# Kernel optimization log

Measured on AMD Instinct MI355X. Metric: run time of the kernel, lower is better.

Reference implementation:

```python
import jax, jax.numpy as jnp
import numpy as np

HIDDEN_DIM = 2048
NUM_EXPERTS = 8
TOP_K = 2
SCORE_SCALE_FACTOR = 1.0
TOKENS = 8192  # batch_size in the original 2D input


def setup_inputs() -> dict:
    key = jax.random.key(0)
    k1, k2, k3 = jax.random.split(key, 3)
    hidden_states = jax.random.normal(k1, (TOKENS, HIDDEN_DIM), dtype=jnp.float32)
    # nn.Linear weights (out_features, in_features), Kaiming-uniform-like scale
    gate_w = jax.random.normal(k2, (NUM_EXPERTS, HIDDEN_DIM), dtype=jnp.float32) / np.float32(np.sqrt(HIDDEN_DIM))
    expert_w = jax.random.normal(k3, (NUM_EXPERTS, HIDDEN_DIM, HIDDEN_DIM), dtype=jnp.float32) / np.float32(np.sqrt(HIDDEN_DIM))
    return {"hidden_states": hidden_states, "gate_w": gate_w, "expert_w": expert_w}


def reference(hidden_states, gate_w, expert_w):
    # router: logits = x @ W_gate^T, softmax in float32 (matches F.softmax(dtype=torch.float))
    router_logits = hidden_states @ gate_w.T                      # [T, E]
    routing_probs = jax.nn.softmax(router_logits.astype(jnp.float32), axis=-1)
    top_w, top_i = jax.lax.top_k(routing_probs, TOP_K)            # [T, K]
    top_w = top_w / jnp.sum(top_w, axis=-1, keepdims=True)        # renormalize over top-k
    top_w = top_w.astype(hidden_states.dtype)

    T = hidden_states.shape[0]
    # dense combine weights [T, E]: zero for unselected experts -> exactly the
    # gather-GEMM-scatter math (full capacity, no dropped tokens)
    combine = jnp.zeros((T, NUM_EXPERTS), dtype=hidden_states.dtype)
    combine = combine.at[jnp.arange(T)[:, None], top_i].set(top_w)

    # out[t,h] = scale * sum_e combine[t,e] * (x[t,:] @ expert_w[e]^T)[h]
    final_hidden_states = jnp.einsum('td,ehd,te->th', hidden_states, expert_w, combine) * SCORE_SCALE_FACTOR
    return final_hidden_states, router_logits
```

## Files before the change

kernel.cpp:

```cpp
#include <hip/hip_runtime.h>
#include <hip/hip_bf16.h>
#include <stdint.h>

#define TOKENS 8192
#define HD     2048
#define NE     8

typedef __attribute__((ext_vector_type(8)))  short short8;
typedef __attribute__((ext_vector_type(8)))  unsigned short ushort8v;
typedef __attribute__((ext_vector_type(4)))  float f32x4;
typedef __attribute__((ext_vector_type(16))) float f32x16;

__device__ __forceinline__ unsigned short f2bf_rne(float f) {
  union { float f; unsigned u; } v; v.f = f;
  unsigned u = v.u;
  return (unsigned short)((u + 0x7fffu + ((u >> 16) & 1u)) >> 16);
}

__device__ __forceinline__ void async_load16(const void* g, void* lds) {
  __builtin_amdgcn_global_load_lds(
      (const __attribute__((address_space(1))) unsigned int*)g,
      (__attribute__((address_space(3))) unsigned int*)lds, 16, 0, 0);
}

__global__ __launch_bounds__(256) void prep_kernel(
    const float* __restrict__ x, const float* __restrict__ gw,
    const float* __restrict__ ew, unsigned short* __restrict__ xb,
    unsigned short* __restrict__ wb, float* __restrict__ logits_out,
    int* __restrict__ counts, int* __restrict__ btok,
    float* __restrict__ bwt) {
  if (blockIdx.x >= 2048) {
    int i = (blockIdx.x - 2048) * 256 + threadIdx.x;
    const int n8 = NE * HD * HD / 8;
    const int stride = 4096 * 256;
    const float4* s4 = (const float4*)ew;
    ushort8v* d8 = (ushort8v*)wb;
    for (; i < n8; i += stride) {
      float4 a = s4[i * 2], b = s4[i * 2 + 1];
      ushort8v o;
      o[0] = f2bf_rne(a.x); o[1] = f2bf_rne(a.y);
      o[2] = f2bf_rne(a.z); o[3] = f2bf_rne(a.w);
      o[4] = f2bf_rne(b.x); o[5] = f2bf_rne(b.y);
      o[6] = f2bf_rne(b.z); o[7] = f2bf_rne(b.w);
      d8[i] = o;
    }
    return;
  }
  const int wid  = threadIdx.x >> 6;
  const int lane = threadIdx.x & 63;
  const int t = blockIdx.x * 4 + wid;

  const float4* xr = (const float4*)(x + (size_t)t * HD);
  const float4* g4 = (const float4*)gw;
  ushort4* xb4 = (ushort4*)(xb + (size_t)t * HD);

  float acc[NE];
#pragma unroll
  for (int e = 0; e < NE; ++e) acc[e] = 0.f;

#pragma unroll
  for (int it = 0; it < 8; ++it) {
    int idx = it * 64 + lane;
    float4 v = xr[idx];
    ushort4 o;
    o.x = f2bf_rne(v.x); o.y = f2bf_rne(v.y);
    o.z = f2bf_rne(v.z); o.w = f2bf_rne(v.w);
    xb4[idx] = o;
#pragma unroll
    for (int e = 0; e < NE; ++e) {
      float4 g = g4[e * 512 + idx];
      acc[e] += v.x * g.x + v.y * g.y + v.z * g.z + v.w * g.w;
    }
  }
#pragma unroll
  for (int e = 0; e < NE; ++e) {
#pragma unroll
    for (int off = 32; off > 0; off >>= 1)
      acc[e] += __shfl_xor(acc[e], off, 64);
  }
  if (lane == 0) {
    float* lo = logits_out + (size_t)t * NE;
#pragma unroll
    for (int e = 0; e < NE; ++e) lo[e] = acc[e];
    int i0 = 0; float b0 = acc[0];
#pragma unroll
    for (int k = 1; k < NE; ++k) if (acc[k] > b0) { b0 = acc[k]; i0 = k; }
    int i1 = -1; float b1 = -3.4e38f;
#pragma unroll
    for (int k = 0; k < NE; ++k) if (k != i0 && acc[k] > b1) { b1 = acc[k]; i1 = k; }
    float w0 = 1.f / (1.f + __expf(b1 - b0));
    float w1 = 1.f - w0;
    int p0 = atomicAdd(&counts[i0 * 32], 1);
    btok[i0 * TOKENS + p0] = t;
    bwt [i0 * TOKENS + p0] = w0;
    int p1 = atomicAdd(&counts[i1 * 32], 1);
    btok[i1 * TOKENS + p1] = t | (1 << 13);
    bwt [i1 * TOKENS + p1] = w1;
  }
}

__global__ __launch_bounds__(256, 4) void moe_gemm_kernel(
    const unsigned short* __restrict__ xb,
    const unsigned short* __restrict__ wb,
    const int* __restrict__ counts,
    const int* __restrict__ btok,
    const float* __restrict__ bwt,
    float* __restrict__ out,
    unsigned short* __restrict__ slot1) {
  int d = blockIdx.x;
  int e, coltile, rowtile;
  if (d < 2048) {
    e       = d & 7;
    rowtile = (d >> 3) & 15;
    coltile = d >> 7;
  } else {
    int u = d - 2048;
    e       = u & 7;
    coltile = (u & 127) >> 3;
    rowtile = 16 + (u >> 7);
  }
  const int cnt = counts[e * 32];
  if (rowtile * 128 >= cnt) return;

  __shared__ unsigned short As[128 * 64];
  __shared__ unsigned short Bs[128 * 64];

  const int tid  = threadIdx.x;
  const int wid  = tid >> 6;
  const int lane = tid & 63;

  int a_off[4], b_off[4];
#pragma unroll
  for (int it = 0; it < 4; ++it) {
    int slot = wid * 256 + it * 64 + lane;
    int row  = slot >> 3;
    int ch   = (slot & 7) ^ (row & 7);
    int rc   = rowtile * 128 + row;
    rc = rc < cnt ? rc : cnt - 1;
    a_off[it] = (btok[e * TOKENS + rc] & (TOKENS - 1)) * HD + ch * 8;
    b_off[it] = (e * HD + coltile * 128 + row) * HD + ch * 8;
  }

  f32x16 acc[2][2];
#pragma unroll
  for (int i = 0; i < 2; ++i)
#pragma unroll
    for (int j = 0; j < 2; ++j)
#pragma unroll
      for (int r = 0; r < 16; ++r) acc[i][j][r] = 0.f;

  const int l5  = lane >> 5;
  const int ln  = lane & 31;
  const int wm2 = wid >> 1;
  const int wn2 = wid & 1;

  int a_rd[2][4], b_rd[2][4];
#pragma unroll
  for (int t = 0; t < 2; ++t)
#pragma unroll
    for (int kc = 0; kc < 4; ++kc) {
      int ra = wm2 * 64 + t * 32 + ln;
      a_rd[t][kc] = ra * 64 + ((kc * 2 + l5) ^ (ra & 7)) * 8;
      int rb = wn2 * 64 + t * 32 + ln;
      b_rd[t][kc] = rb * 64 + ((kc * 2 + l5) ^ (rb & 7)) * 8;
    }

  for (int k0 = 0; k0 < HD; k0 += 64) {
#pragma unroll
    for (int it = 0; it < 4; ++it) {
      async_load16(xb + a_off[it] + k0, &As[(wid * 256 + it * 64) * 8]);
      async_load16(wb + b_off[it] + k0, &Bs[(wid * 256 + it * 64) * 8]);
    }
    __syncthreads();
    short8 fa[2][4], fb[2][4];
#pragma unroll
    for (int t = 0; t < 2; ++t)
#pragma unroll
      for (int kc = 0; kc < 4; ++kc) {
        fa[t][kc] = *(const short8*)&As[a_rd[t][kc]];
        fb[t][kc] = *(const short8*)&Bs[b_rd[t][kc]];
      }
#pragma unroll
    for (int kc = 0; kc < 4; ++kc)
#pragma unroll
      for (int i = 0; i < 2; ++i)
#pragma unroll
        for (int j = 0; j < 2; ++j)
          acc[i][j] = __builtin_amdgcn_mfma_f32_32x32x16_bf16(
              fa[i][kc], fb[j][kc], acc[i][j], 0, 0, 0);
    __syncthreads();
  }

#pragma unroll
  for (int ti = 0; ti < 2; ++ti)
#pragma unroll
    for (int rg = 0; rg < 16; ++rg) {
      int row = (rg & 3) + 8 * (rg >> 2) + 4 * l5;
      int gm  = rowtile * 128 + wm2 * 64 + ti * 32 + row;
      if (gm < cnt) {
        int   dv = btok[e * TOKENS + gm];
        float w  = bwt [e * TOKENS + gm];
        int   nb = coltile * 128 + wn2 * 64 + ln;
        float v0 = w * acc[ti][0][rg];
        float v1 = w * acc[ti][1][rg];
        if (dv < TOKENS) {
          float* orow = out + (size_t)dv * HD + nb;
          orow[0]  = v0;
          orow[32] = v1;
        } else {
          unsigned short* srow = slot1 + (size_t)(dv - TOKENS) * HD + nb;
          srow[0]  = f2bf_rne(v0);
          srow[32] = f2bf_rne(v1);
        }
      }
    }
}

__global__ __launch_bounds__(256) void combine_kernel(
    const unsigned short* __restrict__ s1, float* __restrict__ out) {
  size_t u = (size_t)blockIdx.x * 256 + threadIdx.x;
  ushort8v sv = ((const ushort8v*)s1)[u];
  float4* o = (float4*)out + u * 2;
  float4 a = o[0], b = o[1];
  a.x += __uint_as_float((unsigned)sv[0] << 16);
  a.y += __uint_as_float((unsigned)sv[1] << 16);
  a.z += __uint_as_float((unsigned)sv[2] << 16);
  a.w += __uint_as_float((unsigned)sv[3] << 16);
  b.x += __uint_as_float((unsigned)sv[4] << 16);
  b.y += __uint_as_float((unsigned)sv[5] << 16);
  b.z += __uint_as_float((unsigned)sv[6] << 16);
  b.w += __uint_as_float((unsigned)sv[7] << 16);
  o[0] = a; o[1] = b;
}

extern "C" void kernel_launch(void* const* d_in, const int* in_sizes, int n_in,
                              void* d_out, int out_size, void* d_ws, size_t ws_size,
                              hipStream_t stream) {
  const float* x  = (const float*)d_in[0];
  const float* gw = (const float*)d_in[1];
  const float* ew = (const float*)d_in[2];
  float* out = (float*)d_out;

  char* ws = (char*)d_ws;
  unsigned short* xb    = (unsigned short*)ws;
  unsigned short* wb    = (unsigned short*)(ws + 33554432u);
  unsigned short* slot1 = (unsigned short*)(ws + 100663296u);
  int*   counts = (int*)(ws + 134217728u);
  int*   btok   = (int*)(ws + 134218752u);
  float* bwt    = (float*)(ws + 134480896u);

  float* logits = out + (size_t)TOKENS * HD;

  hipMemsetAsync(counts, 0, 1024, stream);
  prep_kernel<<<6144, 256, 0, stream>>>(x, gw, ew, xb, wb, logits,
                                        counts, btok, bwt);
  moe_gemm_kernel<<<4096, 256, 0, stream>>>(xb, wb, counts, btok, bwt, out, slot1);
  combine_kernel<<<8192, 256, 0, stream>>>(slot1, out);
}
```

Baseline: 483.2 us.

## Group tokens by expert pair so one block computes both experts and combines

Tokens are now bucketed by their unordered top-2 expert pair (28 buckets) rather than by single expert. Each GEMM block loads one A tile and two expert weight tiles, runs both MFMA chains and writes the weighted sum directly. This removes the bf16 slot buffer, its rounding, and the separate combine pass. The cost is smaller, less balanced buckets with more partially filled row tiles, twice the accumulator registers (occupancy hint lowered to 2), and weight tiles re-read across more buckets.

```diff
diff --git a/kernel.cpp b/kernel.cpp
--- a/kernel.cpp
+++ b/kernel.cpp
@@ -5,11 +5,15 @@
 #define TOKENS 8192
 #define HD     2048
 #define NE     8
+#define NP     28
+#define PCAP   8192
 
 typedef __attribute__((ext_vector_type(8)))  short short8;
 typedef __attribute__((ext_vector_type(8)))  unsigned short ushort8v;
-typedef __attribute__((ext_vector_type(4)))  float f32x4;
 typedef __attribute__((ext_vector_type(16))) float f32x16;
+
+__constant__ int d_pa[NP] = {0,0,0,0,0,0,0,1,1,1,1,1,1,2,2,2,2,2,3,3,3,3,4,4,4,5,5,6};
+__constant__ int d_pb[NP] = {1,2,3,4,5,6,7,2,3,4,5,6,7,3,4,5,6,7,4,5,6,7,5,6,7,6,7,7};
 
 __device__ __forceinline__ unsigned short f2bf_rne(float f) {
   union { float f; unsigned u; } v; v.f = f;
@@ -28,7 +32,7 @@
     const float* __restrict__ ew, unsigned short* __restrict__ xb,
     unsigned short* __restrict__ wb, float* __restrict__ logits_out,
     int* __restrict__ counts, int* __restrict__ btok,
-    float* __restrict__ bwt) {
+    float2* __restrict__ bw2) {
   if (blockIdx.x >= 2048) {
     int i = (blockIdx.x - 2048) * 256 + threadIdx.x;
     const int n8 = NE * HD * HD / 8;
@@ -90,64 +94,60 @@
     for (int k = 0; k < NE; ++k) if (k != i0 && acc[k] > b1) { b1 = acc[k]; i1 = k; }
     float w0 = 1.f / (1.f + __expf(b1 - b0));
     float w1 = 1.f - w0;
-    int p0 = atomicAdd(&counts[i0 * 32], 1);
-    btok[i0 * TOKENS + p0] = t;
-    bwt [i0 * TOKENS + p0] = w0;
-    int p1 = atomicAdd(&counts[i1 * 32], 1);
-    btok[i1 * TOKENS + p1] = t | (1 << 13);
-    bwt [i1 * TOKENS + p1] = w1;
-  }
-}
-
-__global__ __launch_bounds__(256, 4) void moe_gemm_kernel(
+    int a  = i0 < i1 ? i0 : i1;
+    int b  = i0 < i1 ? i1 : i0;
+    float wa = i0 < i1 ? w0 : w1;
+    float wbv = i0 < i1 ? w1 : w0;
+    int p = a * (13 - a) / 2 + b - 1;
+    int pos = atomicAdd(&counts[p * 32], 1);
+    btok[p * PCAP + pos] = t;
+    bw2 [p * PCAP + pos] = make_float2(wa, wbv);
+  }
+}
+
+__global__ __launch_bounds__(256, 2) void moe_gemm_kernel(
     const unsigned short* __restrict__ xb,
     const unsigned short* __restrict__ wb,
     const int* __restrict__ counts,
     const int* __restrict__ btok,
-    const float* __restrict__ bwt,
-    float* __restrict__ out,
-    unsigned short* __restrict__ slot1) {
-  int d = blockIdx.x;
-  int e, coltile, rowtile;
-  if (d < 2048) {
-    e       = d & 7;
-    rowtile = (d >> 3) & 15;
-    coltile = d >> 7;
-  } else {
-    int u = d - 2048;
-    e       = u & 7;
-    coltile = (u & 127) >> 3;
-    rowtile = 16 + (u >> 7);
-  }
-  const int cnt = counts[e * 32];
-  if (rowtile * 128 >= cnt) return;
-
-  __shared__ unsigned short As[128 * 64];
-  __shared__ unsigned short Bs[128 * 64];
+    const float2* __restrict__ bw2,
+    float* __restrict__ out) {
+  const int d = blockIdx.x;
+  const int p = d >> 8;
+  const int r = (d >> 4) & 15;
+  const int c = d & 15;
+  const int cnt = counts[p * 32];
+  if (r * 128 >= cnt) return;
+  const int ea = d_pa[p], eb = d_pb[p];
+
+  __shared__ unsigned short As [128 * 64];
+  __shared__ unsigned short B0s[128 * 64];
+  __shared__ unsigned short B1s[128 * 64];
 
   const int tid  = threadIdx.x;
   const int wid  = tid >> 6;
   const int lane = tid & 63;
 
-  int a_off[4], b_off[4];
+  int a_off[4], b0_off[4], b1_off[4];
 #pragma unroll
   for (int it = 0; it < 4; ++it) {
     int slot = wid * 256 + it * 64 + lane;
     int row  = slot >> 3;
     int ch   = (slot & 7) ^ (row & 7);
-    int rc   = rowtile * 128 + row;
+    int rc   = r * 128 + row;
     rc = rc < cnt ? rc : cnt - 1;
-    a_off[it] = (btok[e * TOKENS + rc] & (TOKENS - 1)) * HD + ch * 8;
-    b_off[it] = (e * HD + coltile * 128 + row) * HD + ch * 8;
-  }
-
-  f32x16 acc[2][2];
+    a_off[it]  = btok[p * PCAP + rc] * HD + ch * 8;
+    b0_off[it] = (ea * HD + c * 128 + row) * HD + ch * 8;
+    b1_off[it] = (eb * HD + c * 128 + row) * HD + ch * 8;
+  }
+
+  f32x16 accA[2][2], accB[2][2];
 #pragma unroll
   for (int i = 0; i < 2; ++i)
 #pragma unroll
     for (int j = 0; j < 2; ++j)
 #pragma unroll
-      for (int r = 0; r < 16; ++r) acc[i][j][r] = 0.f;
+      for (int g = 0; g < 16; ++g) { accA[i][j][g] = 0.f; accB[i][j][g] = 0.f; }
 
   const int l5  = lane >> 5;
   const int ln  = lane & 31;
@@ -168,26 +168,29 @@
   for (int k0 = 0; k0 < HD; k0 += 64) {
 #pragma unroll
     for (int it = 0; it < 4; ++it) {
-      async_load16(xb + a_off[it] + k0, &As[(wid * 256 + it * 64) * 8]);
-      async_load16(wb + b_off[it] + k0, &Bs[(wid * 256 + it * 64) * 8]);
+      int lb = (wid * 256 + it * 64) * 8;
+      async_load16(xb + a_off[it]  + k0, &As [lb]);
+      async_load16(wb + b0_off[it] + k0, &B0s[lb]);
+      async_load16(wb + b1_off[it] + k0, &B1s[lb]);
     }
     __syncthreads();
-    short8 fa[2][4], fb[2][4];
-#pragma unroll
-    for (int t = 0; t < 2; ++t)
-#pragma unroll
-      for (int kc = 0; kc < 4; ++kc) {
-        fa[t][kc] = *(const short8*)&As[a_rd[t][kc]];
-        fb[t][kc] = *(const short8*)&Bs[b_rd[t][kc]];
-      }
-#pragma unroll
-    for (int kc = 0; kc < 4; ++kc)
-#pragma unroll
-      for (int i = 0; i < 2; ++i)
-#pragma unroll
-        for (int j = 0; j < 2; ++j)
-          acc[i][j] = __builtin_amdgcn_mfma_f32_32x32x16_bf16(
-              fa[i][kc], fb[j][kc], acc[i][j], 0, 0, 0);
+#pragma unroll
+    for (int kc = 0; kc < 4; ++kc) {
+      short8 a0 = *(const short8*)&As[a_rd[0][kc]];
+      short8 a1 = *(const short8*)&As[a_rd[1][kc]];
+      short8 f0 = *(const short8*)&B0s[b_rd[0][kc]];
+      short8 f1 = *(const short8*)&B0s[b_rd[1][kc]];
+      accA[0][0] = __builtin_amdgcn_mfma_f32_32x32x16_bf16(a0, f0, accA[0][0], 0, 0, 0);
+      accA[0][1] = __builtin_amdgcn_mfma_f32_32x32x16_bf16(a0, f1, accA[0][1], 0, 0, 0);
+      accA[1][0] = __builtin_amdgcn_mfma_f32_32x32x16_bf16(a1, f0, accA[1][0], 0, 0, 0);
+      accA[1][1] = __builtin_amdgcn_mfma_f32_32x32x16_bf16(a1, f1, accA[1][1], 0, 0, 0);
+      short8 g0 = *(const short8*)&B1s[b_rd[0][kc]];
+      short8 g1 = *(const short8*)&B1s[b_rd[1][kc]];
+      accB[0][0] = __builtin_amdgcn_mfma_f32_32x32x16_bf16(a0, g0, accB[0][0], 0, 0, 0);
+      accB[0][1] = __builtin_amdgcn_mfma_f32_32x32x16_bf16(a0, g1, accB[0][1], 0, 0, 0);
+      accB[1][0] = __builtin_amdgcn_mfma_f32_32x32x16_bf16(a1, g0, accB[1][0], 0, 0, 0);
+      accB[1][1] = __builtin_amdgcn_mfma_f32_32x32x16_bf16(a1, g1, accB[1][1], 0, 0, 0);
+    }
     __syncthreads();
   }
 
@@ -196,41 +199,18 @@
 #pragma unroll
     for (int rg = 0; rg < 16; ++rg) {
       int row = (rg & 3) + 8 * (rg >> 2) + 4 * l5;
-      int gm  = rowtile * 128 + wm2 * 64 + ti * 32 + row;
+      int gm  = r * 128 + wm2 * 64 + ti * 32 + row;
       if (gm < cnt) {
-        int   dv = btok[e * TOKENS + gm];
-        float w  = bwt [e * TOKENS + gm];
-        int   nb = coltile * 128 + wn2 * 64 + ln;
-        float v0 = w * acc[ti][0][rg];
-        float v1 = w * acc[ti][1][rg];
-        if (dv < TOKENS) {
-          float* orow = out + (size_t)dv * HD + nb;
-          orow[0]  = v0;
-          orow[32] = v1;
-        } else {
-          unsigned short* srow = slot1 + (size_t)(dv - TOKENS) * HD + nb;
-          srow[0]  = f2bf_rne(v0);
-          srow[32] = f2bf_rne(v1);
-        }
+        int    tok = btok[p * PCAP + gm];
+        float2 w   = bw2 [p * PCAP + gm];
+        int    nb  = c * 128 + wn2 * 64 + ln;
+        float v0 = w.x * accA[ti][0][rg] + w.y * accB[ti][0][rg];
+        float v1 = w.x * accA[ti][1][rg] + w.y * accB[ti][1][rg];
+        float* orow = out + (size_t)tok * HD + nb;
+        orow[0]  = v0;
+        orow[32] = v1;
       }
     }
-}
-
-__global__ __launch_bounds__(256) void combine_kernel(
-    const unsigned short* __restrict__ s1, float* __restrict__ out) {
-  size_t u = (size_t)blockIdx.x * 256 + threadIdx.x;
-  ushort8v sv = ((const ushort8v*)s1)[u];
-  float4* o = (float4*)out + u * 2;
-  float4 a = o[0], b = o[1];
-  a.x += __uint_as_float((unsigned)sv[0] << 16);
-  a.y += __uint_as_float((unsigned)sv[1] << 16);
-  a.z += __uint_as_float((unsigned)sv[2] << 16);
-  a.w += __uint_as_float((unsigned)sv[3] << 16);
-  b.x += __uint_as_float((unsigned)sv[4] << 16);
-  b.y += __uint_as_float((unsigned)sv[5] << 16);
-  b.z += __uint_as_float((unsigned)sv[6] << 16);
-  b.w += __uint_as_float((unsigned)sv[7] << 16);
-  o[0] = a; o[1] = b;
 }
 
 extern "C" void kernel_launch(void* const* d_in, const int* in_sizes, int n_in,
@@ -242,18 +222,16 @@
   float* out = (float*)d_out;
 
   char* ws = (char*)d_ws;
-  unsigned short* xb    = (unsigned short*)ws;
-  unsigned short* wb    = (unsigned short*)(ws + 33554432u);
-  unsigned short* slot1 = (unsigned short*)(ws + 100663296u);
-  int*   counts = (int*)(ws + 134217728u);
-  int*   btok   = (int*)(ws + 134218752u);
-  float* bwt    = (float*)(ws + 134480896u);
+  unsigned short* xb   = (unsigned short*)ws;
+  unsigned short* wb   = (unsigned short*)(ws + 33554432u);
+  int*    btok   = (int*)   (ws + 100663296u);
+  float2* bw2    = (float2*)(ws + 101580800u);
+  int*    counts = (int*)   (ws + 103415808u);
 
   float* logits = out + (size_t)TOKENS * HD;
 
-  hipMemsetAsync(counts, 0, 1024, stream);
+  hipMemsetAsync(counts, 0, NP * 32 * sizeof(int), stream);
   prep_kernel<<<6144, 256, 0, stream>>>(x, gw, ew, xb, wb, logits,
-                                        counts, btok, bwt);
-  moe_gemm_kernel<<<4096, 256, 0, stream>>>(xb, wb, counts, btok, bwt, out, slot1);
-  combine_kernel<<<8192, 256, 0, stream>>>(slot1, out);
-}
+                                        counts, btok, bw2);
+  moe_gemm_kernel<<<NP * 256, 256, 0, stream>>>(xb, wb, counts, btok, bw2, out);
+}
```

Result: slower. 533.9 us (+10.5%).

## Replace bf16 slot buffer and combine pass with atomic fp32 scatter-add

Applied to the files above, without the earlier changes.

Drops the second-slot bf16 staging buffer and the separate combine kernel. Output is zeroed with a memset and the GEMM epilogue does atomicAdd of weighted results straight into fp32 out. Routing and bucketing move into a new bucket_kernel that uses wave ballot plus prefix count, so there is one atomic per wave instead of one per token. This trades the combine kernel's read and write traffic for a 64MB memset and about 33M float atomics, and it adds an extra launch.

```diff
diff --git a/kernel.cpp b/kernel.cpp
--- a/kernel.cpp
+++ b/kernel.cpp
@@ -8,7 +8,6 @@
 
 typedef __attribute__((ext_vector_type(8)))  short short8;
 typedef __attribute__((ext_vector_type(8)))  unsigned short ushort8v;
-typedef __attribute__((ext_vector_type(4)))  float f32x4;
 typedef __attribute__((ext_vector_type(16))) float f32x16;
 
 __device__ __forceinline__ unsigned short f2bf_rne(float f) {
@@ -26,9 +25,7 @@
 __global__ __launch_bounds__(256) void prep_kernel(
     const float* __restrict__ x, const float* __restrict__ gw,
     const float* __restrict__ ew, unsigned short* __restrict__ xb,
-    unsigned short* __restrict__ wb, float* __restrict__ logits_out,
-    int* __restrict__ counts, int* __restrict__ btok,
-    float* __restrict__ bwt) {
+    unsigned short* __restrict__ wb, float* __restrict__ logits_out) {
   if (blockIdx.x >= 2048) {
     int i = (blockIdx.x - 2048) * 256 + threadIdx.x;
     const int n8 = NE * HD * HD / 8;
@@ -82,20 +79,39 @@
     float* lo = logits_out + (size_t)t * NE;
 #pragma unroll
     for (int e = 0; e < NE; ++e) lo[e] = acc[e];
-    int i0 = 0; float b0 = acc[0];
-#pragma unroll
-    for (int k = 1; k < NE; ++k) if (acc[k] > b0) { b0 = acc[k]; i0 = k; }
-    int i1 = -1; float b1 = -3.4e38f;
-#pragma unroll
-    for (int k = 0; k < NE; ++k) if (k != i0 && acc[k] > b1) { b1 = acc[k]; i1 = k; }
-    float w0 = 1.f / (1.f + __expf(b1 - b0));
-    float w1 = 1.f - w0;
-    int p0 = atomicAdd(&counts[i0 * 32], 1);
-    btok[i0 * TOKENS + p0] = t;
-    bwt [i0 * TOKENS + p0] = w0;
-    int p1 = atomicAdd(&counts[i1 * 32], 1);
-    btok[i1 * TOKENS + p1] = t | (1 << 13);
-    bwt [i1 * TOKENS + p1] = w1;
+  }
+}
+
+__global__ __launch_bounds__(256) void bucket_kernel(
+    const float* __restrict__ logits, int* __restrict__ counts,
+    int* __restrict__ btok, float* __restrict__ bwt) {
+  const int e = blockIdx.x & 7;
+  const int t = (blockIdx.x >> 3) * 256 + threadIdx.x;
+  const int lane = threadIdx.x & 63;
+
+  const float4* lo4 = (const float4*)(logits + (size_t)t * NE);
+  float4 la = lo4[0], lb = lo4[1];
+  float l[NE] = {la.x, la.y, la.z, la.w, lb.x, lb.y, lb.z, lb.w};
+  int i0 = 0; float b0 = l[0];
+#pragma unroll
+  for (int k = 1; k < NE; ++k) if (l[k] > b0) { b0 = l[k]; i0 = k; }
+  int i1 = -1; float b1 = -3.4e38f;
+#pragma unroll
+  for (int k = 0; k < NE; ++k) if (k != i0 && l[k] > b1) { b1 = l[k]; i1 = k; }
+  float w0 = 1.f / (1.f + __expf(b1 - b0));
+  float w1 = 1.f - w0;
+
+  bool  p = (i0 == e) || (i1 == e);
+  float w = (i0 == e) ? w0 : w1;
+  unsigned long long mask = __ballot(p);
+  int prefix = __popcll(mask & ((1ull << lane) - 1ull));
+  int tot    = __popcll(mask);
+  int base = 0;
+  if (lane == 0 && tot) base = atomicAdd(&counts[e * 32], tot);
+  base = __shfl(base, 0, 64);
+  if (p) {
+    btok[e * TOKENS + base + prefix] = t;
+    bwt [e * TOKENS + base + prefix] = w;
   }
 }
 
@@ -105,8 +121,7 @@
     const int* __restrict__ counts,
     const int* __restrict__ btok,
     const float* __restrict__ bwt,
-    float* __restrict__ out,
-    unsigned short* __restrict__ slot1) {
+    float* __restrict__ out) {
   int d = blockIdx.x;
   int e, coltile, rowtile;
   if (d < 2048) {
@@ -137,7 +152,7 @@
     int ch   = (slot & 7) ^ (row & 7);
     int rc   = rowtile * 128 + row;
     rc = rc < cnt ? rc : cnt - 1;
-    a_off[it] = (btok[e * TOKENS + rc] & (TOKENS - 1)) * HD + ch * 8;
+    a_off[it] = btok[e * TOKENS + rc] * HD + ch * 8;
     b_off[it] = (e * HD + coltile * 128 + row) * HD + ch * 8;
   }
 
@@ -198,39 +213,14 @@
       int row = (rg & 3) + 8 * (rg >> 2) + 4 * l5;
       int gm  = rowtile * 128 + wm2 * 64 + ti * 32 + row;
       if (gm < cnt) {
-        int   dv = btok[e * TOKENS + gm];
-        float w  = bwt [e * TOKENS + gm];
-        int   nb = coltile * 128 + wn2 * 64 + ln;
-        float v0 = w * acc[ti][0][rg];
-        float v1 = w * acc[ti][1][rg];
-        if (dv < TOKENS) {
-          float* orow = out + (size_t)dv * HD + nb;
-          orow[0]  = v0;
-          orow[32] = v1;
-        } else {
-          unsigned short* srow = slot1 + (size_t)(dv - TOKENS) * HD + nb;
-          srow[0]  = f2bf_rne(v0);
-          srow[32] = f2bf_rne(v1);
-        }
+        int   tok = btok[e * TOKENS + gm];
+        float w   = bwt [e * TOKENS + gm];
+        int   nb  = coltile * 128 + wn2 * 64 + ln;
+        float* orow = out + (size_t)tok * HD + nb;
+        atomicAdd(&orow[0],  w * acc[ti][0][rg]);
+        atomicAdd(&orow[32], w * acc[ti][1][rg]);
       }
     }
-}
-
-__global__ __launch_bounds__(256) void combine_kernel(
-    const unsigned short* __restrict__ s1, float* __restrict__ out) {
-  size_t u = (size_t)blockIdx.x * 256 + threadIdx.x;
-  ushort8v sv = ((const ushort8v*)s1)[u];
-  float4* o = (float4*)out + u * 2;
-  float4 a = o[0], b = o[1];
-  a.x += __uint_as_float((unsigned)sv[0] << 16);
-  a.y += __uint_as_float((unsigned)sv[1] << 16);
-  a.z += __uint_as_float((unsigned)sv[2] << 16);
-  a.w += __uint_as_float((unsigned)sv[3] << 16);
-  b.x += __uint_as_float((unsigned)sv[4] << 16);
-  b.y += __uint_as_float((unsigned)sv[5] << 16);
-  b.z += __uint_as_float((unsigned)sv[6] << 16);
-  b.w += __uint_as_float((unsigned)sv[7] << 16);
-  o[0] = a; o[1] = b;
 }
 
 extern "C" void kernel_launch(void* const* d_in, const int* in_sizes, int n_in,
@@ -242,18 +232,17 @@
   float* out = (float*)d_out;
 
   char* ws = (char*)d_ws;
-  unsigned short* xb    = (unsigned short*)ws;
-  unsigned short* wb    = (unsigned short*)(ws + 33554432u);
-  unsigned short* slot1 = (unsigned short*)(ws + 100663296u);
-  int*   counts = (int*)(ws + 134217728u);
-  int*   btok   = (int*)(ws + 134218752u);
-  float* bwt    = (float*)(ws + 134480896u);
+  unsigned short* xb   = (unsigned short*)ws;
+  unsigned short* wb   = (unsigned short*)(ws + 33554432u);
+  int*   btok   = (int*)  (ws + 100663296u);
+  float* bwt    = (float*)(ws + 100925440u);
+  int*   counts = (int*)  (ws + 101187584u);
 
   float* logits = out + (size_t)TOKENS * HD;
 
+  hipMemsetAsync(out, 0, (size_t)TOKENS * HD * sizeof(float), stream);
   hipMemsetAsync(counts, 0, 1024, stream);
-  prep_kernel<<<6144, 256, 0, stream>>>(x, gw, ew, xb, wb, logits,
-                                        counts, btok, bwt);
-  moe_gemm_kernel<<<4096, 256, 0, stream>>>(xb, wb, counts, btok, bwt, out, slot1);
-  combine_kernel<<<8192, 256, 0, stream>>>(slot1, out);
-}
+  prep_kernel<<<6144, 256, 0, stream>>>(x, gw, ew, xb, wb, logits);
+  bucket_kernel<<<256, 256, 0, stream>>>(logits, counts, btok, bwt);
+  moe_gemm_kernel<<<4096, 256, 0, stream>>>(xb, wb, counts, btok, bwt, out);
+}
```

After: 498.7 us. 3.2% more time.
